# Optimization experiments

Hardware: AMD Instinct MI355X
Metric: run time of the kernel (lower is better)

The kernel has to match this reference:

```python
import jax, jax.numpy as jnp
import numpy as np

N = 65536      # total nodes = B * MAXN
E = 524288     # edges (avg degree 8)
DX = 32; DG = 32
IN_DIM = DX + 3 * DG   # 128, after concat(x, g0, g1, g2)
H = 256; OUT = 8; MAXN = 8192


def setup_inputs() -> dict:
    key = jax.random.key(0)
    ks = jax.random.split(key, 40)
    inp = {}
    inp['x'] = jax.random.normal(ks[0], (N, DX), jnp.float32)
    inp['g0'] = jax.random.normal(ks[1], (N, DG), jnp.float32)
    inp['g1'] = jax.random.normal(ks[2], (N, DG), jnp.float32)
    inp['g2'] = jax.random.normal(ks[3], (N, DG), jnp.float32)
    inp['edge_src'] = jax.random.randint(ks[4], (E,), 0, N, jnp.int32)
    inp['edge_dst'] = jax.random.randint(ks[5], (E,), 0, N, jnp.int32)
    dims = [(IN_DIM, H), (H, H), (H, H), (H, H)]
    k = 6
    for i, (di, do) in enumerate(dims):
        s = 1.0 / np.sqrt(di)
        inp[f'Wl{i}'] = jax.random.uniform(ks[k], (di, do), jnp.float32, -s, s); k += 1
        inp[f'Wr{i}'] = jax.random.uniform(ks[k], (di, do), jnp.float32, -s, s); k += 1
        inp[f'b{i}'] = jnp.zeros((do,), jnp.float32)
    s = 1.0 / np.sqrt(MAXN)
    inp['mlp1_W1'] = jax.random.uniform(ks[k], (MAXN, H), jnp.float32, -s, s); k += 1
    inp['mlp1_b1'] = jnp.zeros((H,), jnp.float32)
    s = 1.0 / np.sqrt(H)
    inp['mlp1_W2'] = jax.random.uniform(ks[k], (H, 1), jnp.float32, -s, s); k += 1
    inp['mlp1_b2'] = jnp.zeros((1,), jnp.float32)
    inp['bn_gamma'] = jnp.ones((H,), jnp.float32)
    inp['bn_beta'] = jnp.zeros((H,), jnp.float32)
    inp['mlp2_W1'] = jax.random.uniform(ks[k], (H, H), jnp.float32, -s, s); k += 1
    inp['mlp2_b1'] = jnp.zeros((H,), jnp.float32)
    inp['mlp2_W2'] = jax.random.uniform(ks[k], (H, OUT), jnp.float32, -s, s); k += 1
    inp['mlp2_b2'] = jnp.zeros((OUT,), jnp.float32)
    return inp


def _forward(x, g0, g1, g2, edge_src, edge_dst,
             Wl0, Wr0, b0, Wl1, Wr1, b1, Wl2, Wr2, b2, Wl3, Wr3, b3,
             mlp1_W1, mlp1_b1, mlp1_W2, mlp1_b2, bn_gamma, bn_beta,
             mlp2_W1, mlp2_b1, mlp2_W2, mlp2_b2):
    h = jnp.concatenate([x, g0, g1, g2], axis=1)  # [N, IN_DIM]
    # mean-aggregation denominator (in-degree, clamped at 1 like PyG mean)
    cnt = jnp.maximum(
        jax.ops.segment_sum(jnp.ones((E,), h.dtype), edge_dst, num_segments=N), 1.0)
    for Wl, Wr, b in ((Wl0, Wr0, b0), (Wl1, Wr1, b1), (Wl2, Wr2, b2), (Wl3, Wr3, b3)):
        agg = jax.ops.segment_sum(h[edge_src], edge_dst, num_segments=N) / cnt[:, None]
        # SAGEConv: lin_l(mean of neighbors) + lin_r(self) + bias, then ReLU
        h = jax.nn.relu(agg @ Wl + h @ Wr + b)
        # F.dropout in eval / deterministic reference: identity
    h = h.reshape(-1, H, MAXN)                               # [B, H, MAXN]
    h = jax.nn.relu(jnp.einsum('bhm,mk->bhk', h, mlp1_W1) + mlp1_b1)
    h = (jnp.einsum('bhk,ko->bho', h, mlp1_W2) + mlp1_b2)[..., 0]  # [B, H]
    mean = h.mean(axis=0)
    var = h.var(axis=0)
    h = (h - mean) / jnp.sqrt(var + 1e-5) * bn_gamma + bn_beta
    h = jax.nn.relu(h)
    h = jax.nn.relu(h @ mlp2_W1 + mlp2_b1)
    return h @ mlp2_W2 + mlp2_b2                              # [B, OUT]


def reference(x, g0, g1, g2, edge_src, edge_dst,
              Wl0, Wr0, b0, Wl1, Wr1, b1, Wl2, Wr2, b2, Wl3, Wr3, b3,
              mlp1_W1, mlp1_b1, mlp1_W2, mlp1_b2, bn_gamma, bn_beta,
              mlp2_W1, mlp2_b1, mlp2_W2, mlp2_b2):
    return _forward(x, g0, g1, g2, edge_src, edge_dst,
                    Wl0, Wr0, b0, Wl1, Wr1, b1, Wl2, Wr2, b2, Wl3, Wr3, b3,
                    mlp1_W1, mlp1_b1, mlp1_W2, mlp1_b2, bn_gamma, bn_beta,
                    mlp2_W1, mlp2_b1, mlp2_W2, mlp2_b2)
```

## Files before the change

### kernel.cpp

```cpp
#include <hip/hip_runtime.h>
#include <hip/hip_bf16.h>


#define NN 65536
#define EE 524288
#define ROWS 65537
#define PCSR_CAP 720896

using frag16 = __attribute__((ext_vector_type(8))) short;
using f32x4  = __attribute__((ext_vector_type(4))) float;

__device__ __forceinline__ float b2f(unsigned short u) {
    union { unsigned u32; float f; } x; x.u32 = (unsigned)u << 16; return x.f;
}

__device__ __forceinline__ void gld_lds16(const void* g, void* l) {
    __builtin_amdgcn_global_load_lds(
        (const __attribute__((address_space(1))) void*)g,
        (__attribute__((address_space(3))) void*)l, 16, 0, 0);
}


__global__ void gs_zero_deg(int* deg) {
    int i = blockIdx.x * 256 + threadIdx.x;
    if (i < NN) deg[i] = 0;
}

__global__ void gs_hist(const int* __restrict__ dst, int* __restrict__ deg) {
    int e = blockIdx.x * 256 + threadIdx.x;
    atomicAdd(&deg[dst[e]], 1);
}

__global__ void gs_deg_reduce(const int* __restrict__ deg, int* __restrict__ bsum) {
    int t = threadIdx.x;
    int p = (deg[blockIdx.x * 256 + t] + 3) & ~3;
#pragma unroll
    for (int off = 32; off > 0; off >>= 1) p += __shfl_down(p, off);
    __shared__ int w4[4];
    if ((t & 63) == 0) w4[t >> 6] = p;
    __syncthreads();
    if (t == 0) bsum[blockIdx.x] = w4[0] + w4[1] + w4[2] + w4[3];
}

__global__ void gs_scan_bsum(const int* __restrict__ bsum, int* __restrict__ bofs,
                             int* __restrict__ prow) {
    __shared__ int part[256];
    int t = threadIdx.x;
    int v = bsum[t];
    part[t] = v;
    __syncthreads();
    for (int off = 1; off < 256; off <<= 1) {
        int add = (t >= off) ? part[t - off] : 0;
        __syncthreads();
        part[t] += add;
        __syncthreads();
    }
    bofs[t] = part[t] - v;
    if (t == 255) prow[NN] = part[255];
}

__global__ void gs_scan_apply(const int* __restrict__ deg, const int* __restrict__ bofs,
                              int* __restrict__ prow, int* __restrict__ cursor,
                              float* __restrict__ inv_cnt, int* __restrict__ pcsr,
                              __hip_bfloat16* __restrict__ P0,
                              __hip_bfloat16* __restrict__ P1) {
    __shared__ int part[256];
    int t = threadIdx.x;
    int i = blockIdx.x * 256 + t;
    int d = deg[i];
    int p = (d + 3) & ~3;
    part[t] = p;
    __syncthreads();
    for (int off = 1; off < 256; off <<= 1) {
        int add = (t >= off) ? part[t - off] : 0;
        __syncthreads();
        part[t] += add;
        __syncthreads();
    }
    int beg = bofs[blockIdx.x] + part[t] - p;
    prow[i] = beg;
    cursor[i] = beg;
    inv_cnt[i] = 1.0f / (float)(d > 0 ? d : 1);
    for (int j = d; j < p; ++j) pcsr[beg + j] = NN;
    if (blockIdx.x == 0) {
        ((unsigned*)(P0 + (size_t)NN * 512))[t] = 0u;
        ((unsigned*)(P1 + (size_t)NN * 512))[t] = 0u;
    }
}

__global__ void gs_bucket(const int* __restrict__ src, const int* __restrict__ dst,
                          int* __restrict__ cursor, int* __restrict__ pcsr) {
    int e = blockIdx.x * 256 + threadIdx.x;
    int d = dst[e];
    int p = atomicAdd(&cursor[d], 1);
    pcsr[p] = src[e];
}

struct TcvtArgs {
    const float* src[8];
    __hip_bfloat16* dst[8];
    int ldk[8];
    int kofs[8];
    int kblk[8];
};

__global__ void gs_tcvt_all(TcvtArgs a) {
    int z = blockIdx.z;
    if ((int)blockIdx.x >= a.kblk[z]) return;
    const float* src = a.src[z];
    __hip_bfloat16* dst = a.dst[z];
    int ldk = a.ldk[z], kofs = a.kofs[z];
    __shared__ float tile[32][33];
    int kb = blockIdx.x * 32, nb = blockIdx.y * 32;
    int tx = threadIdx.x, ty = threadIdx.y;
#pragma unroll
    for (int i = 0; i < 32; i += 8)
        tile[ty + i][tx] = src[(size_t)(kb + ty + i) * 256 + nb + tx];
    __syncthreads();
#pragma unroll
    for (int i = 0; i < 32; i += 8) {
        int n = nb + ty + i, k = kb + tx;
        dst[(size_t)n * ldk + kofs + k] = __float2bfloat16(tile[tx][ty + i]);
    }
}

__global__ void gs_tcvt(const float* __restrict__ src, __hip_bfloat16* __restrict__ dst,
                        int ldk, int kofs) {
    __shared__ float tile[32][33];
    int kb = blockIdx.x * 32, nb = blockIdx.y * 32;
    int tx = threadIdx.x, ty = threadIdx.y;
#pragma unroll
    for (int i = 0; i < 32; i += 8)
        tile[ty + i][tx] = src[(size_t)(kb + ty + i) * 256 + nb + tx];
    __syncthreads();
#pragma unroll
    for (int i = 0; i < 32; i += 8) {
        int n = nb + ty + i, k = kb + tx;
        dst[(size_t)n * ldk + kofs + k] = __float2bfloat16(tile[tx][ty + i]);
    }
}

__global__ void gs_concat_bf(const float* __restrict__ x, const float* __restrict__ g0,
                             const float* __restrict__ g1, const float* __restrict__ g2,
                             __hip_bfloat16* __restrict__ h) {
    int idx = blockIdx.x * 256 + threadIdx.x;
    int n = idx >> 7, c = idx & 127;
    float v;
    if (c < 32)       v = x[n * 32 + c];
    else if (c < 64)  v = g0[n * 32 + (c - 32)];
    else if (c < 96)  v = g1[n * 32 + (c - 64)];
    else              v = g2[n * 32 + (c - 96)];
    h[(size_t)n * 512 + 256 + c] = __float2bfloat16(v);
}

template <int DIM>
__global__ void gs_agg_bf(const __hip_bfloat16* __restrict__ hsrc,
                          __hip_bfloat16* __restrict__ adst,
                          const int* __restrict__ prow, const int* __restrict__ pcsr,
                          const float* __restrict__ inv_cnt) {
    int wave = threadIdx.x >> 6;
    int lane = threadIdx.x & 63;
    int n = blockIdx.x * 4 + wave;
    int e = prow[n], pe = prow[n + 1];
    float iv = inv_cnt[n];
    if constexpr (DIM == 256) {
        const __hip_bfloat16* base = hsrc + lane * 4;
        float a0 = 0.f, a1 = 0.f, a2 = 0.f, a3 = 0.f;
        int4 s4;
        if (e < pe) s4 = *(const int4*)(pcsr + e);
        while (e < pe) {
            int4 cur = s4;
            e += 4;
            if (e < pe) s4 = *(const int4*)(pcsr + e);
            ushort4 v0 = *(const ushort4*)(base + (size_t)cur.x * 512);
            ushort4 v1 = *(const ushort4*)(base + (size_t)cur.y * 512);
            ushort4 v2 = *(const ushort4*)(base + (size_t)cur.z * 512);
            ushort4 v3 = *(const ushort4*)(base + (size_t)cur.w * 512);
            a0 += b2f(v0.x); a1 += b2f(v0.y); a2 += b2f(v0.z); a3 += b2f(v0.w);
            a0 += b2f(v1.x); a1 += b2f(v1.y); a2 += b2f(v1.z); a3 += b2f(v1.w);
            a0 += b2f(v2.x); a1 += b2f(v2.y); a2 += b2f(v2.z); a3 += b2f(v2.w);
            a0 += b2f(v3.x); a1 += b2f(v3.y); a2 += b2f(v3.z); a3 += b2f(v3.w);
        }
        __hip_bfloat16 o[4] = {__float2bfloat16(a0 * iv), __float2bfloat16(a1 * iv),
                               __float2bfloat16(a2 * iv), __float2bfloat16(a3 * iv)};
        *(ushort4*)(adst + (size_t)n * 512 + lane * 4) = *(const ushort4*)o;
    } else {
        const __hip_bfloat16* base = hsrc + lane * 2;
        float a0 = 0.f, a1 = 0.f;
        int4 s4;
        if (e < pe) s4 = *(const int4*)(pcsr + e);
        while (e < pe) {
            int4 cur = s4;
            e += 4;
            if (e < pe) s4 = *(const int4*)(pcsr + e);
            ushort2 v0 = *(const ushort2*)(base + (size_t)cur.x * 512);
            ushort2 v1 = *(const ushort2*)(base + (size_t)cur.y * 512);
            ushort2 v2 = *(const ushort2*)(base + (size_t)cur.z * 512);
            ushort2 v3 = *(const ushort2*)(base + (size_t)cur.w * 512);
            a0 += b2f(v0.x); a1 += b2f(v0.y);
            a0 += b2f(v1.x); a1 += b2f(v1.y);
            a0 += b2f(v2.x); a1 += b2f(v2.y);
            a0 += b2f(v3.x); a1 += b2f(v3.y);
        }
        __hip_bfloat16 o[2] = {__float2bfloat16(a0 * iv), __float2bfloat16(a1 * iv)};
        *(ushort2*)(adst + (size_t)n * 512 + lane * 2) = *(const ushort2*)o;
    }
}

__device__ __forceinline__ void mfma_block(const __hip_bfloat16* A, int lda,
                                           const __hip_bfloat16* Bt, int ldb,
                                           int kbeg, int kend, size_t row0, size_t nbase,
                                           __hip_bfloat16* As, __hip_bfloat16* Bs,
                                           f32x4 acc[4][4]) {
    const int t = threadIdx.x;
    const int lane = t & 63;
    const int w = t >> 6;
    const int wr = (w >> 1) * 64;
    const int wc = (w & 1) * 64;
    const int srow = w * 32 + (lane >> 3);
    const int scol = (lane & 7) * 8;
    for (int kc = kbeg; kc < kend; kc += 64) {
#pragma unroll
        for (int l = 0; l < 4; ++l) {
            gld_lds16(A + (row0 + srow + 8 * l) * (size_t)lda + kc + scol,
                      As + (w * 32 + 8 * l) * 64);
            gld_lds16(Bt + (nbase + srow + 8 * l) * (size_t)ldb + kc + scol,
                      Bs + (w * 32 + 8 * l) * 64);
        }
        __syncthreads();
#pragma unroll
        for (int kk = 0; kk < 64; kk += 32) {
            frag16 af[4], bf[4];
#pragma unroll
            for (int i = 0; i < 4; ++i)
                af[i] = *(const frag16*)(As + (wr + i * 16 + (lane & 15)) * 64 + kk + (lane >> 4) * 8);
#pragma unroll
            for (int j = 0; j < 4; ++j)
                bf[j] = *(const frag16*)(Bs + (wc + j * 16 + (lane & 15)) * 64 + kk + (lane >> 4) * 8);
#pragma unroll
            for (int i = 0; i < 4; ++i)
#pragma unroll
                for (int j = 0; j < 4; ++j)
                    acc[i][j] = __builtin_amdgcn_mfma_f32_16x16x32_bf16(af[i], bf[j], acc[i][j], 0, 0, 0);
        }
        __syncthreads();
    }
}

__global__ __launch_bounds__(256, 2)
void gs_gemm_bias_relu(const __hip_bfloat16* __restrict__ A, int lda, int K,
                       const __hip_bfloat16* __restrict__ Bt, int ldb,
                       const float* __restrict__ bias,
                       __hip_bfloat16* __restrict__ C, int ldc, int cofs) {
    __shared__ __hip_bfloat16 As[128 * 64];
    __shared__ __hip_bfloat16 Bs[128 * 64];
    f32x4 acc[4][4] = {};
    const size_t row0 = (size_t)blockIdx.x * 128;
    const size_t nbase = (size_t)blockIdx.y * 128;
    mfma_block(A, lda, Bt, ldb, 0, K, row0, nbase, As, Bs, acc);
    const int lane = threadIdx.x & 63;
    const int w = threadIdx.x >> 6;
    const int wr = (w >> 1) * 64, wc = (w & 1) * 64;
#pragma unroll
    for (int j = 0; j < 4; ++j) {
        int n = (int)nbase + wc + j * 16 + (lane & 15);
        float bv = bias[n];
#pragma unroll
        for (int i = 0; i < 4; ++i) {
#pragma unroll
            for (int r = 0; r < 4; ++r) {
                size_t row = row0 + wr + i * 16 + (lane >> 4) * 4 + r;
                C[row * (size_t)ldc + cofs + n] = __float2bfloat16(fmaxf(acc[i][j][r] + bv, 0.f));
            }
        }
    }
}

__global__ __launch_bounds__(256, 2)
void gs_gemm_splitk(const __hip_bfloat16* __restrict__ A, int lda,
                    const __hip_bfloat16* __restrict__ Bt, int ldb,
                    float* __restrict__ part) {
    __shared__ __hip_bfloat16 As[128 * 64];
    __shared__ __hip_bfloat16 Bs[128 * 64];
    f32x4 acc[4][4] = {};
    const size_t row0 = (size_t)blockIdx.x * 128;
    const size_t nbase = (size_t)blockIdx.y * 128;
    const int kbeg = blockIdx.z * 512;
    mfma_block(A, lda, Bt, ldb, kbeg, kbeg + 512, row0, nbase, As, Bs, acc);
    const int lane = threadIdx.x & 63;
    const int w = threadIdx.x >> 6;
    const int wr = (w >> 1) * 64, wc = (w & 1) * 64;
    float* p = part + (size_t)blockIdx.z * 2048 * 256;
#pragma unroll
    for (int j = 0; j < 4; ++j) {
        int n = (int)nbase + wc + j * 16 + (lane & 15);
#pragma unroll
        for (int i = 0; i < 4; ++i) {
#pragma unroll
            for (int r = 0; r < 4; ++r) {
                size_t row = row0 + wr + i * 16 + (lane >> 4) * 4 + r;
                p[row * 256 + n] = acc[i][j][r];
            }
        }
    }
}

__global__ void gs_mlp1_reduce(const float* __restrict__ part, const float* __restrict__ b1,
                               float* __restrict__ t1) {
    int idx = blockIdx.x * 256 + threadIdx.x;
    float s = 0.f;
#pragma unroll
    for (int ks = 0; ks < 16; ++ks) s += part[(size_t)ks * 524288 + idx];
    s += b1[idx & 255];
    t1[idx] = fmaxf(s, 0.f);
}

__global__ void gs_pool(const float* __restrict__ t1, const float* __restrict__ W2,
                        const float* __restrict__ b2, float* __restrict__ pooled) {
    int r = blockIdx.x;
    int l = threadIdx.x;
    float acc = 0.f;
#pragma unroll
    for (int q = 0; q < 4; ++q) {
        int c = l + q * 64;
        acc = fmaf(t1[(size_t)r * 256 + c], W2[c], acc);
    }
    for (int off = 32; off > 0; off >>= 1) acc += __shfl_down(acc, off);
    if (l == 0) pooled[r] = acc + b2[0];
}

__global__ void gs_bn_mlp2(const float* __restrict__ pooled, const float* __restrict__ gamma,
                           const float* __restrict__ beta, const float* __restrict__ W1,
                           const float* __restrict__ b1, const float* __restrict__ W2,
                           const float* __restrict__ b2, float* __restrict__ out) {
    __shared__ float hb[8][256];
    __shared__ float h2[8][256];
    int t = threadIdx.x;
    {
        float v[8];
        float m = 0.f;
#pragma unroll
        for (int b = 0; b < 8; ++b) { v[b] = pooled[b * 256 + t]; m += v[b]; }
        m *= 0.125f;
        float var = 0.f;
#pragma unroll
        for (int b = 0; b < 8; ++b) { float d = v[b] - m; var += d * d; }
        var *= 0.125f;
        float is = 1.0f / sqrtf(var + 1e-5f);
        float g = gamma[t], bt = beta[t];
#pragma unroll
        for (int b = 0; b < 8; ++b) hb[b][t] = fmaxf((v[b] - m) * is * g + bt, 0.f);
    }
    __syncthreads();
    {
        float acc[8] = {};
        for (int i = 0; i < 256; ++i) {
            float w = W1[i * 256 + t];
#pragma unroll
            for (int b = 0; b < 8; ++b) acc[b] = fmaf(hb[b][i], w, acc[b]);
        }
        float bb = b1[t];
#pragma unroll
        for (int b = 0; b < 8; ++b) h2[b][t] = fmaxf(acc[b] + bb, 0.f);
    }
    __syncthreads();
    if (t < 64) {
        int b = t >> 3, o = t & 7;
        float acc = 0.f;
        for (int j = 0; j < 256; ++j) acc = fmaf(h2[b][j], W2[j * 8 + o], acc);
        out[b * 8 + o] = acc + b2[o];
    }
}

extern "C" void kernel_launch(void* const* d_in, const int* in_sizes, int n_in,
                              void* d_out, int out_size, void* d_ws, size_t ws_size,
                              hipStream_t stream) {
    const float* x  = (const float*)d_in[0];
    const float* g0 = (const float*)d_in[1];
    const float* g1 = (const float*)d_in[2];
    const float* g2 = (const float*)d_in[3];
    const int* edge_src = (const int*)d_in[4];
    const int* edge_dst = (const int*)d_in[5];
    const float* Wl[4] = {(const float*)d_in[6], (const float*)d_in[9],
                          (const float*)d_in[12], (const float*)d_in[15]};
    const float* Wr[4] = {(const float*)d_in[7], (const float*)d_in[10],
                          (const float*)d_in[13], (const float*)d_in[16]};
    const float* bs[4] = {(const float*)d_in[8], (const float*)d_in[11],
                          (const float*)d_in[14], (const float*)d_in[17]};
    const float* mlp1_W1 = (const float*)d_in[18];
    const float* mlp1_b1 = (const float*)d_in[19];
    const float* mlp1_W2 = (const float*)d_in[20];
    const float* mlp1_b2 = (const float*)d_in[21];
    const float* bn_gamma = (const float*)d_in[22];
    const float* bn_beta  = (const float*)d_in[23];
    const float* mlp2_W1 = (const float*)d_in[24];
    const float* mlp2_b1 = (const float*)d_in[25];
    const float* mlp2_W2 = (const float*)d_in[26];
    const float* mlp2_b2 = (const float*)d_in[27];
    float* out = (float*)d_out;

    char* ws = (char*)d_ws;
    __hip_bfloat16* P0 = (__hip_bfloat16*)ws;
    __hip_bfloat16* P1 = P0 + (size_t)ROWS * 512;
    __hip_bfloat16* WC0 = P1 + (size_t)ROWS * 512;
    __hip_bfloat16* WC1 = WC0 + 65536;
    __hip_bfloat16* WC2 = WC1 + 131072;
    __hip_bfloat16* WC3 = WC2 + 131072;
    __hip_bfloat16* W1T = WC3 + 131072;
    float* inv_cnt = (float*)(W1T + 2097152);
    int* ideg = (int*)(inv_cnt + 65536);
    int* prow = ideg + 65536;
    int* cursor = prow + 65544;
    int* bsum = cursor + 65536;
    int* bofs = bsum + 256;
    int* pcsr = bofs + 256;
    __hip_bfloat16* H4 = P0;
    float* T1 = (float*)P1;
    float* pooled = T1 + 524288;
    float* PART = (float*)((char*)P1 + (size_t)(4 << 20));

    gs_zero_deg<<<256, 256, 0, stream>>>(ideg);
    gs_hist<<<EE / 256, 256, 0, stream>>>(edge_dst, ideg);
    gs_deg_reduce<<<256, 256, 0, stream>>>(ideg, bsum);
    gs_scan_bsum<<<1, 256, 0, stream>>>(bsum, bofs, prow);
    gs_scan_apply<<<256, 256, 0, stream>>>(ideg, bofs, prow, cursor, inv_cnt, pcsr, P0, P1);
    gs_bucket<<<EE / 256, 256, 0, stream>>>(edge_src, edge_dst, cursor, pcsr);

    {
        TcvtArgs a;
        const float* srcs[8] = {Wl[0], Wr[0], Wl[1], Wr[1], Wl[2], Wr[2], Wl[3], Wr[3]};
        __hip_bfloat16* dsts[8] = {WC0, WC0, WC1, WC1, WC2, WC2, WC3, WC3};
        int ldks[8] = {256, 256, 512, 512, 512, 512, 512, 512};
        int kofss[8] = {0, 128, 0, 256, 0, 256, 0, 256};
        int kblks[8] = {4, 4, 8, 8, 8, 8, 8, 8};
        for (int i = 0; i < 8; ++i) {
            a.src[i] = srcs[i]; a.dst[i] = dsts[i];
            a.ldk[i] = ldks[i]; a.kofs[i] = kofss[i]; a.kblk[i] = kblks[i];
        }
        gs_tcvt_all<<<dim3(8, 8, 8), dim3(32, 8), 0, stream>>>(a);
    }
    gs_tcvt<<<dim3(256, 8), dim3(32, 8), 0, stream>>>(mlp1_W1, W1T, 8192, 0);

    gs_concat_bf<<<NN * 128 / 256, 256, 0, stream>>>(x, g0, g1, g2, P0);

    gs_agg_bf<128><<<NN / 4, 256, 0, stream>>>(P0 + 256, P0 + 128, prow, pcsr, inv_cnt);
    gs_gemm_bias_relu<<<dim3(NN / 128, 2), 256, 0, stream>>>(P0 + 128, 512, 256, WC0, 256,
                                                             bs[0], P1, 512, 256);
    gs_agg_bf<256><<<NN / 4, 256, 0, stream>>>(P1 + 256, P1, prow, pcsr, inv_cnt);
    gs_gemm_bias_relu<<<dim3(NN / 128, 2), 256, 0, stream>>>(P1, 512, 512, WC1, 512,
                                                             bs[1], P0, 512, 256);
    gs_agg_bf<256><<<NN / 4, 256, 0, stream>>>(P0 + 256, P0, prow, pcsr, inv_cnt);
    gs_gemm_bias_relu<<<dim3(NN / 128, 2), 256, 0, stream>>>(P0, 512, 512, WC2, 512,
                                                             bs[2], P1, 512, 256);
    gs_agg_bf<256><<<NN / 4, 256, 0, stream>>>(P1 + 256, P1, prow, pcsr, inv_cnt);
    gs_gemm_bias_relu<<<dim3(NN / 128, 2), 256, 0, stream>>>(P1, 512, 512, WC3, 512,
                                                             bs[3], H4, 256, 0);

    gs_gemm_splitk<<<dim3(16, 2, 16), 256, 0, stream>>>(H4, 8192, W1T, 8192, PART);
    gs_mlp1_reduce<<<2048, 256, 0, stream>>>(PART, mlp1_b1, T1);
    gs_pool<<<2048, 64, 0, stream>>>(T1, mlp1_W2, mlp1_b2, pooled);

    gs_bn_mlp2<<<1, 256, 0, stream>>>(pooled, bn_gamma, bn_beta, mlp2_W1, mlp2_b1,
                                      mlp2_W2, mlp2_b2, out);
}
```

Baseline: 497.7 us.

## Vectorize aggregation, concat and GEMM epilogues; fuse MLP1 reduce with pooling

The aggregation kernel now splits each wave into two halves that gather alternate neighbours with 16-byte loads and combine them with a cross-half shuffle. To support this, CSR rows are padded to multiples of 8 and the CSR capacity is raised. The MFMA operand order is swapped so each lane holds four consecutive output columns, which lets the GEMM and split-K epilogues use vector stores. Concat reads float4 per thread, and the split-K reduce is fused with the pooling dot product so the T1 intermediate is no longer written. In exchange, more padded edge slots are gathered from the zero row.

```diff
diff --git a/kernel.cpp b/kernel.cpp
--- a/kernel.cpp
+++ b/kernel.cpp
@@ -5,10 +5,12 @@
 #define NN 65536
 #define EE 524288
 #define ROWS 65537
-#define PCSR_CAP 720896
+#define PCSR_CAP 983040
 
 using frag16 = __attribute__((ext_vector_type(8))) short;
 using f32x4  = __attribute__((ext_vector_type(4))) float;
+using us8    = __attribute__((ext_vector_type(8))) unsigned short;
+using us4v   = __attribute__((ext_vector_type(4))) unsigned short;
 
 __device__ __forceinline__ float b2f(unsigned short u) {
     union { unsigned u32; float f; } x; x.u32 = (unsigned)u << 16; return x.f;
@@ -33,7 +35,7 @@
 
 __global__ void gs_deg_reduce(const int* __restrict__ deg, int* __restrict__ bsum) {
     int t = threadIdx.x;
-    int p = (deg[blockIdx.x * 256 + t] + 3) & ~3;
+    int p = (deg[blockIdx.x * 256 + t] + 7) & ~7;
 #pragma unroll
     for (int off = 32; off > 0; off >>= 1) p += __shfl_down(p, off);
     __shared__ int w4[4];
@@ -68,7 +70,7 @@
     int t = threadIdx.x;
     int i = blockIdx.x * 256 + t;
     int d = deg[i];
-    int p = (d + 3) & ~3;
+    int p = (d + 7) & ~7;
     part[t] = p;
     __syncthreads();
     for (int off = 1; off < 256; off <<= 1) {
@@ -144,13 +146,17 @@
                              const float* __restrict__ g1, const float* __restrict__ g2,
                              __hip_bfloat16* __restrict__ h) {
     int idx = blockIdx.x * 256 + threadIdx.x;
-    int n = idx >> 7, c = idx & 127;
-    float v;
-    if (c < 32)       v = x[n * 32 + c];
-    else if (c < 64)  v = g0[n * 32 + (c - 32)];
-    else if (c < 96)  v = g1[n * 32 + (c - 64)];
-    else              v = g2[n * 32 + (c - 96)];
-    h[(size_t)n * 512 + 256 + c] = __float2bfloat16(v);
+    int n = idx >> 5, q = idx & 31;
+    int c0 = q * 4;
+    const float* src = (c0 < 32) ? (x  + (size_t)n * 32 + c0)
+                     : (c0 < 64) ? (g0 + (size_t)n * 32 + (c0 - 32))
+                     : (c0 < 96) ? (g1 + (size_t)n * 32 + (c0 - 64))
+                                 : (g2 + (size_t)n * 32 + (c0 - 96));
+    f32x4 v = *(const f32x4*)src;
+    union { us4v u; __hip_bfloat16 b[4]; } o;
+#pragma unroll
+    for (int r = 0; r < 4; ++r) o.b[r] = __float2bfloat16(v[r]);
+    *(us4v*)(h + (size_t)n * 512 + 256 + c0) = o.u;
 }
 
 template <int DIM>
@@ -158,52 +164,55 @@
                           __hip_bfloat16* __restrict__ adst,
                           const int* __restrict__ prow, const int* __restrict__ pcsr,
                           const float* __restrict__ inv_cnt) {
+    constexpr int EL = DIM / 32;
     int wave = threadIdx.x >> 6;
     int lane = threadIdx.x & 63;
     int n = blockIdx.x * 4 + wave;
     int e = prow[n], pe = prow[n + 1];
     float iv = inv_cnt[n];
-    if constexpr (DIM == 256) {
-        const __hip_bfloat16* base = hsrc + lane * 4;
-        float a0 = 0.f, a1 = 0.f, a2 = 0.f, a3 = 0.f;
-        int4 s4;
-        if (e < pe) s4 = *(const int4*)(pcsr + e);
-        while (e < pe) {
-            int4 cur = s4;
-            e += 4;
-            if (e < pe) s4 = *(const int4*)(pcsr + e);
-            ushort4 v0 = *(const ushort4*)(base + (size_t)cur.x * 512);
-            ushort4 v1 = *(const ushort4*)(base + (size_t)cur.y * 512);
-            ushort4 v2 = *(const ushort4*)(base + (size_t)cur.z * 512);
-            ushort4 v3 = *(const ushort4*)(base + (size_t)cur.w * 512);
-            a0 += b2f(v0.x); a1 += b2f(v0.y); a2 += b2f(v0.z); a3 += b2f(v0.w);
-            a0 += b2f(v1.x); a1 += b2f(v1.y); a2 += b2f(v1.z); a3 += b2f(v1.w);
-            a0 += b2f(v2.x); a1 += b2f(v2.y); a2 += b2f(v2.z); a3 += b2f(v2.w);
-            a0 += b2f(v3.x); a1 += b2f(v3.y); a2 += b2f(v3.z); a3 += b2f(v3.w);
-        }
-        __hip_bfloat16 o[4] = {__float2bfloat16(a0 * iv), __float2bfloat16(a1 * iv),
-                               __float2bfloat16(a2 * iv), __float2bfloat16(a3 * iv)};
-        *(ushort4*)(adst + (size_t)n * 512 + lane * 4) = *(const ushort4*)o;
-    } else {
-        const __hip_bfloat16* base = hsrc + lane * 2;
-        float a0 = 0.f, a1 = 0.f;
-        int4 s4;
-        if (e < pe) s4 = *(const int4*)(pcsr + e);
-        while (e < pe) {
-            int4 cur = s4;
-            e += 4;
-            if (e < pe) s4 = *(const int4*)(pcsr + e);
-            ushort2 v0 = *(const ushort2*)(base + (size_t)cur.x * 512);
-            ushort2 v1 = *(const ushort2*)(base + (size_t)cur.y * 512);
-            ushort2 v2 = *(const ushort2*)(base + (size_t)cur.z * 512);
-            ushort2 v3 = *(const ushort2*)(base + (size_t)cur.w * 512);
-            a0 += b2f(v0.x); a1 += b2f(v0.y);
-            a0 += b2f(v1.x); a1 += b2f(v1.y);
-            a0 += b2f(v2.x); a1 += b2f(v2.y);
-            a0 += b2f(v3.x); a1 += b2f(v3.y);
-        }
-        __hip_bfloat16 o[2] = {__float2bfloat16(a0 * iv), __float2bfloat16(a1 * iv)};
-        *(ushort2*)(adst + (size_t)n * 512 + lane * 2) = *(const ushort2*)o;
+    const int half = lane >> 5;
+    const __hip_bfloat16* base = hsrc + (lane & 31) * EL;
+    float a[EL];
+#pragma unroll
+    for (int k = 0; k < EL; ++k) a[k] = 0.f;
+    int4 sa, sb;
+    if (e < pe) { sa = *(const int4*)(pcsr + e); sb = *(const int4*)(pcsr + e + 4); }
+    while (e < pe) {
+        int4 ca = sa, cb = sb;
+        e += 8;
+        if (e < pe) { sa = *(const int4*)(pcsr + e); sb = *(const int4*)(pcsr + e + 4); }
+        int r0 = half ? ca.y : ca.x;
+        int r1 = half ? ca.w : ca.z;
+        int r2 = half ? cb.y : cb.x;
+        int r3 = half ? cb.w : cb.z;
+        if constexpr (DIM == 256) {
+            us8 v0 = *(const us8*)(base + (size_t)r0 * 512);
+            us8 v1 = *(const us8*)(base + (size_t)r1 * 512);
+            us8 v2 = *(const us8*)(base + (size_t)r2 * 512);
+            us8 v3 = *(const us8*)(base + (size_t)r3 * 512);
+#pragma unroll
+            for (int k = 0; k < 8; ++k)
+                a[k] += b2f(v0[k]) + b2f(v1[k]) + b2f(v2[k]) + b2f(v3[k]);
+        } else {
+            us4v v0 = *(const us4v*)(base + (size_t)r0 * 512);
+            us4v v1 = *(const us4v*)(base + (size_t)r1 * 512);
+            us4v v2 = *(const us4v*)(base + (size_t)r2 * 512);
+            us4v v3 = *(const us4v*)(base + (size_t)r3 * 512);
+#pragma unroll
+            for (int k = 0; k < 4; ++k)
+                a[k] += b2f(v0[k]) + b2f(v1[k]) + b2f(v2[k]) + b2f(v3[k]);
+        }
+    }
+#pragma unroll
+    for (int k = 0; k < EL; ++k) a[k] += __shfl_xor(a[k], 32);
+    if (half == 0) {
+        union { us8 v8; us4v v4; __hip_bfloat16 b[8]; } o;
+#pragma unroll
+        for (int k = 0; k < EL; ++k) o.b[k] = __float2bfloat16(a[k] * iv);
+        if constexpr (DIM == 256)
+            *(us8*)(adst + (size_t)n * 512 + (lane & 31) * 8) = o.v8;
+        else
+            *(us4v*)(adst + (size_t)n * 512 + (lane & 31) * 4) = o.v4;
     }
 }
 
@@ -241,7 +250,7 @@
             for (int i = 0; i < 4; ++i)
 #pragma unroll
                 for (int j = 0; j < 4; ++j)
-                    acc[i][j] = __builtin_amdgcn_mfma_f32_16x16x32_bf16(af[i], bf[j], acc[i][j], 0, 0, 0);
+                    acc[i][j] = __builtin_amdgcn_mfma_f32_16x16x32_bf16(bf[j], af[i], acc[i][j], 0, 0, 0);
         }
         __syncthreads();
     }
@@ -261,17 +270,20 @@
     const int lane = threadIdx.x & 63;
     const int w = threadIdx.x >> 6;
     const int wr = (w >> 1) * 64, wc = (w & 1) * 64;
+    const int nq = (lane >> 4) * 4;
+    const int ml = lane & 15;
 #pragma unroll
     for (int j = 0; j < 4; ++j) {
-        int n = (int)nbase + wc + j * 16 + (lane & 15);
-        float bv = bias[n];
+        int n0 = (int)nbase + wc + j * 16 + nq;
+        f32x4 bv = *(const f32x4*)(bias + n0);
 #pragma unroll
         for (int i = 0; i < 4; ++i) {
-#pragma unroll
-            for (int r = 0; r < 4; ++r) {
-                size_t row = row0 + wr + i * 16 + (lane >> 4) * 4 + r;
-                C[row * (size_t)ldc + cofs + n] = __float2bfloat16(fmaxf(acc[i][j][r] + bv, 0.f));
-            }
+            size_t row = row0 + wr + i * 16 + ml;
+            union { us4v v; __hip_bfloat16 b[4]; } o;
+#pragma unroll
+            for (int r = 0; r < 4; ++r)
+                o.b[r] = __float2bfloat16(fmaxf(acc[i][j][r] + bv[r], 0.f));
+            *(us4v*)(C + row * (size_t)ldc + cofs + n0) = o.v;
         }
     }
 }
@@ -290,43 +302,35 @@
     const int lane = threadIdx.x & 63;
     const int w = threadIdx.x >> 6;
     const int wr = (w >> 1) * 64, wc = (w & 1) * 64;
+    const int nq = (lane >> 4) * 4;
+    const int ml = lane & 15;
     float* p = part + (size_t)blockIdx.z * 2048 * 256;
 #pragma unroll
     for (int j = 0; j < 4; ++j) {
-        int n = (int)nbase + wc + j * 16 + (lane & 15);
+        int n0 = (int)nbase + wc + j * 16 + nq;
 #pragma unroll
         for (int i = 0; i < 4; ++i) {
-#pragma unroll
-            for (int r = 0; r < 4; ++r) {
-                size_t row = row0 + wr + i * 16 + (lane >> 4) * 4 + r;
-                p[row * 256 + n] = acc[i][j][r];
-            }
-        }
-    }
-}
-
-__global__ void gs_mlp1_reduce(const float* __restrict__ part, const float* __restrict__ b1,
-                               float* __restrict__ t1) {
-    int idx = blockIdx.x * 256 + threadIdx.x;
+            size_t row = row0 + wr + i * 16 + ml;
+            *(f32x4*)(p + row * 256 + n0) = acc[i][j];
+        }
+    }
+}
+
+__global__ void gs_mlp1_pool(const float* __restrict__ part, const float* __restrict__ b1,
+                             const float* __restrict__ W2, const float* __restrict__ b2,
+                             float* __restrict__ pooled) {
+    int r = blockIdx.x;
+    int t = threadIdx.x;
     float s = 0.f;
 #pragma unroll
-    for (int ks = 0; ks < 16; ++ks) s += part[(size_t)ks * 524288 + idx];
-    s += b1[idx & 255];
-    t1[idx] = fmaxf(s, 0.f);
-}
-
-__global__ void gs_pool(const float* __restrict__ t1, const float* __restrict__ W2,
-                        const float* __restrict__ b2, float* __restrict__ pooled) {
-    int r = blockIdx.x;
-    int l = threadIdx.x;
-    float acc = 0.f;
-#pragma unroll
-    for (int q = 0; q < 4; ++q) {
-        int c = l + q * 64;
-        acc = fmaf(t1[(size_t)r * 256 + c], W2[c], acc);
-    }
-    for (int off = 32; off > 0; off >>= 1) acc += __shfl_down(acc, off);
-    if (l == 0) pooled[r] = acc + b2[0];
+    for (int ks = 0; ks < 16; ++ks) s += part[(size_t)ks * 524288 + r * 256 + t];
+    s = fmaxf(s + b1[t], 0.f) * W2[t];
+#pragma unroll
+    for (int off = 32; off > 0; off >>= 1) s += __shfl_down(s, off);
+    __shared__ float w4[4];
+    if ((t & 63) == 0) w4[t >> 6] = s;
+    __syncthreads();
+    if (t == 0) pooled[r] = w4[0] + w4[1] + w4[2] + w4[3] + b2[0];
 }
 
 __global__ void gs_bn_mlp2(const float* __restrict__ pooled, const float* __restrict__ gamma,
@@ -415,8 +419,7 @@
     int* bofs = bsum + 256;
     int* pcsr = bofs + 256;
     __hip_bfloat16* H4 = P0;
-    float* T1 = (float*)P1;
-    float* pooled = T1 + 524288;
+    float* pooled = (float*)P1 + 524288;
     float* PART = (float*)((char*)P1 + (size_t)(4 << 20));
 
     gs_zero_deg<<<256, 256, 0, stream>>>(ideg);
@@ -441,7 +444,7 @@
     }
     gs_tcvt<<<dim3(256, 8), dim3(32, 8), 0, stream>>>(mlp1_W1, W1T, 8192, 0);
 
-    gs_concat_bf<<<NN * 128 / 256, 256, 0, stream>>>(x, g0, g1, g2, P0);
+    gs_concat_bf<<<NN * 32 / 256, 256, 0, stream>>>(x, g0, g1, g2, P0);
 
     gs_agg_bf<128><<<NN / 4, 256, 0, stream>>>(P0 + 256, P0 + 128, prow, pcsr, inv_cnt);
     gs_gemm_bias_relu<<<dim3(NN / 128, 2), 256, 0, stream>>>(P0 + 128, 512, 256, WC0, 256,
@@ -457,8 +460,7 @@
                                                              bs[3], H4, 256, 0);
 
     gs_gemm_splitk<<<dim3(16, 2, 16), 256, 0, stream>>>(H4, 8192, W1T, 8192, PART);
-    gs_mlp1_reduce<<<2048, 256, 0, stream>>>(PART, mlp1_b1, T1);
-    gs_pool<<<2048, 64, 0, stream>>>(T1, mlp1_W2, mlp1_b2, pooled);
+    gs_mlp1_pool<<<2048, 256, 0, stream>>>(PART, mlp1_b1, mlp1_W2, mlp1_b2, pooled);
 
     gs_bn_mlp2<<<1, 256, 0, stream>>>(pooled, bn_gamma, bn_beta, mlp2_W1, mlp2_b1,
                                       mlp2_W2, mlp2_b2, out);
```

Result: slower. 537.5 us (+8.0%).
